# Kernel tuning notes

Measured on AMD Instinct MI355X. Metric: run time of the kernel, lower is better.

## Reference

```python
import jax, jax.numpy as jnp
import numpy as np

D, H, HD, P, IMG, GRID = 768, 12, 64, 16, 224, 14
L = GRID * GRID            # 196 patch tokens
S = L + 1                  # +CLS
LAYERS, FF, OUT, N = 12, 3072, 512, 16
MASKING_BLOCK, LAST_LAYER = 10, 10  # returns at block 11 (= last_layer + 1)
NEG = -1e30


def setup_inputs() -> dict:
    key = jax.random.key(0)
    ks = jax.random.split(key, 20)
    nrm = lambda k, shp, s=0.02: jax.random.normal(k, shp, dtype=jnp.float32) * s
    inp = {}
    inp['masked_img'] = jax.random.normal(ks[0], (N, 3, IMG, IMG), jnp.float32)
    inp['prompted_img'] = jax.random.normal(ks[1], (N, 3, IMG, IMG), jnp.float32)
    # binary segmentation masks (match torch bool-cast semantics in make_attn_mask)
    inp['pred_masks'] = (jax.random.uniform(ks[2], (N, GRID, GRID)) > 0.5).astype(jnp.float32)
    inp['conv_w'] = nrm(ks[3], (D, 3, P, P))
    inp['class_emb'] = nrm(ks[4], (D,))
    inp['pos_emb'] = nrm(ks[5], (S, D))
    inp['ln_pre_g'] = jnp.ones((D,), jnp.float32)
    inp['ln_pre_b'] = jnp.zeros((D,), jnp.float32)
    inp['Wqkv'] = nrm(ks[6], (LAYERS, 3 * D, D))
    inp['bqkv'] = jnp.zeros((LAYERS, 3 * D), jnp.float32)
    inp['Wo'] = nrm(ks[7], (LAYERS, D, D))
    inp['bo'] = jnp.zeros((LAYERS, D), jnp.float32)
    inp['ln1_g'] = jnp.ones((LAYERS, D), jnp.float32)
    inp['ln1_b'] = jnp.zeros((LAYERS, D), jnp.float32)
    inp['ln2_g'] = jnp.ones((LAYERS, D), jnp.float32)
    inp['ln2_b'] = jnp.zeros((LAYERS, D), jnp.float32)
    inp['Wfc'] = nrm(ks[8], (LAYERS, FF, D))
    inp['bfc'] = jnp.zeros((LAYERS, FF), jnp.float32)
    inp['Wp'] = nrm(ks[9], (LAYERS, D, FF))
    inp['bp'] = jnp.zeros((LAYERS, D), jnp.float32)
    inp['ln_post_g'] = jnp.ones((D,), jnp.float32)
    inp['ln_post_b'] = jnp.zeros((D,), jnp.float32)
    inp['proj'] = nrm(ks[10], (D, OUT))
    return inp


def _ln(x, g, b, eps=1e-5):
    mu = jnp.mean(x, axis=-1, keepdims=True)
    var = jnp.mean(jnp.square(x - mu), axis=-1, keepdims=True)
    return (x - mu) * jax.lax.rsqrt(var + eps) * g + b


def _mha(x, Wqkv, bqkv, Wo, bo, bias=None):
    B, Sx, _ = x.shape
    qkv = x @ Wqkv.T + bqkv
    q, k, v = jnp.split(qkv, 3, axis=-1)
    q = q.reshape(B, Sx, H, HD)
    k = k.reshape(B, Sx, H, HD)
    v = v.reshape(B, Sx, H, HD)
    scores = jnp.einsum('bqhd,bkhd->bhqk', q, k) / jnp.sqrt(jnp.float32(HD))
    if bias is not None:
        scores = scores + bias  # bias: [B,1,S,S] broadcast over heads
    a = jax.nn.softmax(scores, axis=-1)
    o = jnp.einsum('bhqk,bkhd->bqhd', a, v).reshape(B, Sx, D)
    return o @ Wo.T + bo


def _embed(img, conv_w, class_emb, pos_emb, ln_pre_g, ln_pre_b):
    feat = jax.lax.conv_general_dilated(
        img, conv_w, window_strides=(P, P), padding='VALID',
        dimension_numbers=('NCHW', 'OIHW', 'NCHW'))  # [B,D,14,14]
    tok = feat.reshape(img.shape[0], D, L).transpose(0, 2, 1)  # [B,L,D]
    cls = jnp.broadcast_to(class_emb, (img.shape[0], 1, D))
    x = jnp.concatenate([cls, tok], axis=1) + pos_emb
    return _ln(x, ln_pre_g, ln_pre_b)


def reference(masked_img, prompted_img, pred_masks, conv_w, class_emb, pos_emb,
              ln_pre_g, ln_pre_b, Wqkv, bqkv, Wo, bo, ln1_g, ln1_b, ln2_g, ln2_b,
              Wfc, bfc, Wp, bp, ln_post_g, ln_post_b, proj):
    def block(x, i, bias=None):
        x = x + _mha(_ln(x, ln1_g[i], ln1_b[i]), Wqkv[i], bqkv[i], Wo[i], bo[i], bias)
        h = _ln(x, ln2_g[i], ln2_b[i]) @ Wfc[i].T + bfc[i]
        h = h * jax.nn.sigmoid(1.702 * h)  # QuickGELU
        return x + h @ Wp[i].T + bp[i]

    x = _embed(masked_img, conv_w, class_emb, pos_emb, ln_pre_g, ln_pre_b)
    x2 = _embed(prompted_img, conv_w, class_emb, pos_emb, ln_pre_g, ln_pre_b)
    x12 = jnp.concatenate([x, x2], axis=0)  # share blocks over both streams
    for i in range(MASKING_BLOCK):
        x12 = block(x12, i)
    n = pred_masks.shape[0]
    x, x2 = x12[:n], x12[n:]
    pm = pred_masks.reshape(n, L, 1)
    # attn mask: only CLS row masked where pred_mask == 0 (True in ~attn_masks -> -inf)
    cls_bias = jnp.where(pred_masks.reshape(n, L) != 0, 0.0, NEG)
    bias = jnp.zeros((n, 1, S, S), jnp.float32).at[:, 0, 0, 1:].set(cls_bias)
    for i in (MASKING_BLOCK, LAST_LAYER + 1):  # blocks 10, 11
        _x2 = jnp.concatenate([x2[:, :1, :], x2[:, 1:, :] * pm], axis=1)  # token masking
        x = block(_x2 * 2.0 + x, i)
        x2 = block(x2, i, bias)
    cls_out = _ln(x[:, 0], ln_post_g, ln_post_b)
    return cls_out @ proj  # [N, 512]
```

## Files before the change

kernel.cpp:

```cpp
#include <hip/hip_runtime.h>
#include <cstdint>
#include <cstddef>

#define D_ 768
#define NH_ 12
#define HD_ 64
#define S_ 197
#define LTOK_ 196
#define FF_ 3072
#define NIMG_ 16
#define OUT_ 512
#define LAYERS_ 12

typedef unsigned short u16;
typedef __bf16 bf16x8 __attribute__((ext_vector_type(8)));
typedef float f32x4 __attribute__((ext_vector_type(4)));
typedef u16 u16x8 __attribute__((ext_vector_type(8)));

__device__ __forceinline__ u16 f2bf(float f) {
  uint32_t u = __builtin_bit_cast(uint32_t, f);
  u = (u + 0x7FFFu + ((u >> 16) & 1u)) >> 16;
  return (u16)u;
}

typedef __attribute__((address_space(3))) void lvoid;
typedef __attribute__((address_space(1))) void gvoid;
__device__ __forceinline__ void async16(const u16* g, u16* l) {
  __builtin_amdgcn_global_load_lds((gvoid*)(uintptr_t)g,
                                   (lvoid*)(uint32_t)(uintptr_t)l, 16, 0, 0);
}

__global__ __launch_bounds__(256) void cvt_kernel(const float* __restrict__ src,
                                                  u16* __restrict__ dst, int n4) {
  int i = blockIdx.x * 256 + threadIdx.x;
  if (i >= n4) return;
  const float4 v = ((const float4*)src)[i];
  ushort4 o;
  o.x = f2bf(v.x); o.y = f2bf(v.y); o.z = f2bf(v.z); o.w = f2bf(v.w);
  ((ushort4*)dst)[i] = o;
}

__global__ __launch_bounds__(256) void im2col_kernel(const float* __restrict__ mimg,
                                                     const float* __restrict__ pimg,
                                                     u16* __restrict__ Xp) {
  const int row = blockIdx.x;
  const int n = row / LTOK_, l = row % LTOK_;
  const float* img = (n < NIMG_) ? (mimg + (size_t)n * 3 * 224 * 224)
                                 : (pimg + (size_t)(n - NIMG_) * 3 * 224 * 224);
  const int gy = l / 14, gx = l % 14;
  for (int col = threadIdx.x; col < D_; col += 256) {
    const int c = col >> 8, py = (col >> 4) & 15, px = col & 15;
    Xp[(size_t)row * D_ + col] = f2bf(img[c * 50176 + (gy * 16 + py) * 224 + gx * 16 + px]);
  }
}

template <int EPI>
__global__ __launch_bounds__(256, 2) void gemm_bt(const u16* __restrict__ A,
                                                  const u16* __restrict__ Bw,
                                                  const float* __restrict__ bias,
                                                  float* __restrict__ Cf,
                                                  u16* __restrict__ Cb,
                                                  int M, int N, int K) {
  __shared__ __align__(16) u16 As[128 * 32];
  __shared__ __align__(16) u16 Bs[128 * 32];
  const int t = threadIdx.x, lane = t & 63, w = t >> 6;
  const int wm = (w >> 1) << 6, wn = (w & 1) << 6;
  const int mBase = blockIdx.y << 7, nBase = blockIdx.x << 7;
  f32x4 acc[4][4];
  const f32x4 z = {0.f, 0.f, 0.f, 0.f};
#pragma unroll
  for (int i = 0; i < 4; i++)
#pragma unroll
    for (int j = 0; j < 4; j++) acc[i][j] = z;

  const int lr = t >> 2, lc = (t & 3) << 3;
  const u16* Ag = A + (size_t)(mBase + lr) * K + lc;
  const u16* Bg = Bw + (size_t)(nBase + lr) * K + lc;
  const size_t halfs = (size_t)64 * K;
  u16* Al = As + t * 8;
  u16* Bl = Bs + t * 8;
  const int q8 = (lane >> 4) << 3, r16 = lane & 15;

  for (int k0 = 0; k0 < K; k0 += 32) {
    async16(Ag, Al);  async16(Ag + halfs, Al + 2048);
    async16(Bg, Bl);  async16(Bg + halfs, Bl + 2048);
    Ag += 32; Bg += 32;
    __syncthreads();
    bf16x8 af[4], bfr[4];
#pragma unroll
    for (int mt = 0; mt < 4; mt++)
      af[mt] = *(const bf16x8*)(As + (wm + mt * 16 + r16) * 32 + q8);
#pragma unroll
    for (int nt = 0; nt < 4; nt++)
      bfr[nt] = *(const bf16x8*)(Bs + (wn + nt * 16 + r16) * 32 + q8);
#pragma unroll
    for (int mt = 0; mt < 4; mt++)
#pragma unroll
      for (int nt = 0; nt < 4; nt++)
        acc[mt][nt] = __builtin_amdgcn_mfma_f32_16x16x32_bf16(af[mt], bfr[nt], acc[mt][nt], 0, 0, 0);
    __syncthreads();
  }

  const int colB = nBase + wn + r16;
  const int rowB = mBase + wm + ((lane >> 4) << 2);
#pragma unroll
  for (int nt = 0; nt < 4; nt++) {
    const int col = colB + nt * 16;
    const float bv = (EPI == 0) ? 0.f : bias[col];
#pragma unroll
    for (int mt = 0; mt < 4; mt++) {
#pragma unroll
      for (int r = 0; r < 4; r++) {
        const int row = rowB + mt * 16 + r;
        const size_t o = (size_t)row * N + col;
        const float v = acc[mt][nt][r];
        if (EPI == 0) {
          Cf[o] = v;
        } else if (EPI == 1) {
          Cb[o] = f2bf(v + bv);
        } else if (EPI == 2) {
          const float hh = v + bv;
          Cb[o] = f2bf(hh / (1.f + __expf(-1.702f * hh)));
        } else {
          Cf[o] += v + bv;
        }
      }
    }
  }
}

__device__ __forceinline__ void st_ln(float* p, float v) { *p = v; }
__device__ __forceinline__ void st_ln(u16* p, float v) { *p = f2bf(v); }

template <typename OT>
__global__ __launch_bounds__(256) void ln_rows(const float* __restrict__ x, size_t strideIn,
                                               OT* __restrict__ y, size_t strideOut,
                                               const float* __restrict__ gw,
                                               const float* __restrict__ bw) {
  const int row = blockIdx.x, t = threadIdx.x;
  const float* xr = x + (size_t)row * strideIn;
  float v0 = xr[t], v1 = xr[t + 256], v2 = xr[t + 512];
  float s1 = v0 + v1 + v2;
  float s2 = v0 * v0 + v1 * v1 + v2 * v2;
#pragma unroll
  for (int off = 1; off < 64; off <<= 1) {
    s1 += __shfl_xor(s1, off);
    s2 += __shfl_xor(s2, off);
  }
  __shared__ float as1[4], as2[4];
  const int lane = t & 63, w = t >> 6;
  if (lane == 0) { as1[w] = s1; as2[w] = s2; }
  __syncthreads();
  s1 = as1[0] + as1[1] + as1[2] + as1[3];
  s2 = as2[0] + as2[1] + as2[2] + as2[3];
  const float mu = s1 * (1.f / 768.f);
  const float rs = rsqrtf(fmaxf(s2 * (1.f / 768.f) - mu * mu, 0.f) + 1e-5f);
  OT* yr = y + (size_t)row * strideOut;
  st_ln(yr + t, (v0 - mu) * rs * gw[t] + bw[t]);
  st_ln(yr + t + 256, (v1 - mu) * rs * gw[t + 256] + bw[t + 256]);
  st_ln(yr + t + 512, (v2 - mu) * rs * gw[t + 512] + bw[t + 512]);
}

__global__ __launch_bounds__(256) void assemble_x(const float* __restrict__ tokf,
                                                  const float* __restrict__ cls,
                                                  const float* __restrict__ pos,
                                                  float* __restrict__ x12) {
  const int row = blockIdx.x;
  const int n = row / S_, s = row % S_;
  for (int d = threadIdx.x; d < D_; d += 256) {
    float v = (s == 0) ? cls[d] : tokf[(size_t)(n * LTOK_ + s - 1) * D_ + d];
    x12[(size_t)row * D_ + d] = v + pos[s * D_ + d];
  }
}

__global__ __launch_bounds__(256) void combine_kernel(float* __restrict__ xa,
                                                      const float* __restrict__ xb,
                                                      const float* __restrict__ pm) {
  const int row = blockIdx.x;
  const int b = row / S_, s = row % S_;
  const float m2 = (s == 0) ? 2.f : 2.f * pm[b * LTOK_ + s - 1];
  for (int d = threadIdx.x; d < D_; d += 256) {
    const size_t o = (size_t)row * D_ + d;
    xa[o] += m2 * xb[o];
  }
}

#define KPAD_ 224
#define VSTR_ 232

__global__ __launch_bounds__(256, 2) void attn_kernel(const u16* __restrict__ qkv,
                                                      u16* __restrict__ out,
                                                      const float* __restrict__ pm,
                                                      int useBias) {
  __shared__ __align__(16) u16 Vt[64 * VSTR_];
  __shared__ __align__(16) u16 Pb4[4 * 16 * VSTR_];
  const int bh = blockIdx.x, b = bh / NH_, h = bh % NH_;
  const int t = threadIdx.x, lane = t & 63, w = t >> 6;
  const int r16 = lane & 15, quad = lane >> 4;

  const u16* Qb = qkv + (size_t)b * S_ * 2304 + h * HD_;
  const u16* Kb = Qb + D_;
  const u16* Vb = Qb + 2 * D_;

#pragma unroll
  for (int it = 0; it < 7; it++) {
    const int lin = it * 256 + t;
    const int col = lin & 63, k0 = (lin >> 6) << 3;
    u16x8 tmp;
#pragma unroll
    for (int j = 0; j < 8; j++) {
      const int key = k0 + j;
      tmp[j] = (key < S_) ? Vb[(size_t)key * 2304 + col] : (u16)0;
    }
    *(u16x8*)&Vt[col * VSTR_ + k0] = tmp;
  }
  __syncthreads();

  u16* Pb = Pb4 + w * (16 * VSTR_);
  const f32x4 z = {0.f, 0.f, 0.f, 0.f};

  for (int it = 0; it < 4; it++) {
    int mt = it * 4 + w;
    const bool real = (mt < 13);
    if (!real) mt = 12;
    const int qbase = mt * 16;

    const u16* qrow = Qb + (size_t)(qbase + r16) * 2304 + quad * 8;
    const bf16x8 a0 = *(const bf16x8*)(qrow);
    const bf16x8 a1 = *(const bf16x8*)(qrow + 32);
    f32x4 c[14];
#pragma unroll
    for (int nt = 0; nt < 14; nt++) {
      const u16* krow = Kb + (size_t)(nt * 16 + r16) * 2304 + quad * 8;
      const bf16x8 b0 = *(const bf16x8*)(krow);
      const bf16x8 b1 = *(const bf16x8*)(krow + 32);
      f32x4 cc = __builtin_amdgcn_mfma_f32_16x16x32_bf16(a0, b0, z, 0, 0, 0);
      c[nt] = __builtin_amdgcn_mfma_f32_16x16x32_bf16(a1, b1, cc, 0, 0, 0);
    }

    float mx[4] = {-3.0e38f, -3.0e38f, -3.0e38f, -3.0e38f};
#pragma unroll
    for (int nt = 0; nt < 14; nt++) {
      const int key = nt * 16 + r16;
      if (key >= S_) {
#pragma unroll
        for (int r = 0; r < 4; r++) c[nt][r] = -1e30f;
      } else {
#pragma unroll
        for (int r = 0; r < 4; r++) c[nt][r] *= 0.125f;
        if (useBias && mt == 0 && quad == 0 && key >= 1)
          c[nt][0] += (pm[b * LTOK_ + key - 1] != 0.f) ? 0.f : -1e30f;
      }
#pragma unroll
      for (int r = 0; r < 4; r++) mx[r] = fmaxf(mx[r], c[nt][r]);
    }
#pragma unroll
    for (int off = 1; off < 16; off <<= 1)
#pragma unroll
      for (int r = 0; r < 4; r++) mx[r] = fmaxf(mx[r], __shfl_xor(mx[r], off));
    float sum[4] = {0.f, 0.f, 0.f, 0.f};
#pragma unroll
    for (int nt = 0; nt < 14; nt++)
#pragma unroll
      for (int r = 0; r < 4; r++) {
        const float e = __expf(c[nt][r] - mx[r]);
        c[nt][r] = e;
        sum[r] += e;
      }
#pragma unroll
    for (int off = 1; off < 16; off <<= 1)
#pragma unroll
      for (int r = 0; r < 4; r++) sum[r] += __shfl_xor(sum[r], off);
    float inv[4];
#pragma unroll
    for (int r = 0; r < 4; r++) inv[r] = 1.f / sum[r];

#pragma unroll
    for (int nt = 0; nt < 14; nt++)
#pragma unroll
      for (int r = 0; r < 4; r++)
        Pb[(quad * 4 + r) * VSTR_ + nt * 16 + r16] = f2bf(c[nt][r] * inv[r]);
    __syncthreads();

    f32x4 ov[4] = {z, z, z, z};
#pragma unroll
    for (int kk = 0; kk < 7; kk++) {
      const bf16x8 pa = *(const bf16x8*)(Pb + r16 * VSTR_ + kk * 32 + quad * 8);
#pragma unroll
      for (int vt = 0; vt < 4; vt++) {
        const bf16x8 vb = *(const bf16x8*)(Vt + (vt * 16 + r16) * VSTR_ + kk * 32 + quad * 8);
        ov[vt] = __builtin_amdgcn_mfma_f32_16x16x32_bf16(pa, vb, ov[vt], 0, 0, 0);
      }
    }
    if (real) {
#pragma unroll
      for (int r = 0; r < 4; r++) {
        const int qq = qbase + quad * 4 + r;
        if (qq < S_) {
#pragma unroll
          for (int vt = 0; vt < 4; vt++)
            out[(size_t)(b * S_ + qq) * D_ + h * HD_ + vt * 16 + r16] = f2bf(ov[vt][r]);
        }
      }
    }
    __syncthreads();
  }
}

__global__ __launch_bounds__(256) void final_proj_kernel(const float* __restrict__ clsn,
                                                         const float* __restrict__ proj,
                                                         float* __restrict__ outp) {
  __shared__ float cs[D_];
  const int b = blockIdx.x;
  for (int d = threadIdx.x; d < D_; d += 256) cs[d] = clsn[b * D_ + d];
  __syncthreads();
  for (int o = threadIdx.x; o < OUT_; o += 256) {
    float acc = 0.f;
    for (int d = 0; d < D_; d++) acc += cs[d] * proj[d * OUT_ + o];
    outp[b * OUT_ + o] = acc;
  }
}

extern "C" void kernel_launch(void* const* d_in, const int* in_sizes, int n_in,
                              void* d_out, int out_size, void* d_ws, size_t ws_size,
                              hipStream_t stream) {
  (void)in_sizes; (void)n_in; (void)out_size; (void)ws_size;
  const float* masked   = (const float*)d_in[0];
  const float* prompted = (const float*)d_in[1];
  const float* pmasks   = (const float*)d_in[2];
  const float* conv_w   = (const float*)d_in[3];
  const float* class_emb= (const float*)d_in[4];
  const float* pos_emb  = (const float*)d_in[5];
  const float* ln_pre_g = (const float*)d_in[6];
  const float* ln_pre_b = (const float*)d_in[7];
  const float* Wqkv     = (const float*)d_in[8];
  const float* bqkv     = (const float*)d_in[9];
  const float* Wo       = (const float*)d_in[10];
  const float* bo       = (const float*)d_in[11];
  const float* ln1_g    = (const float*)d_in[12];
  const float* ln1_b    = (const float*)d_in[13];
  const float* ln2_g    = (const float*)d_in[14];
  const float* ln2_b    = (const float*)d_in[15];
  const float* Wfc      = (const float*)d_in[16];
  const float* bfc      = (const float*)d_in[17];
  const float* Wp       = (const float*)d_in[18];
  const float* bp       = (const float*)d_in[19];
  const float* ln_post_g= (const float*)d_in[20];
  const float* ln_post_b= (const float*)d_in[21];
  const float* projw    = (const float*)d_in[22];

  char* pws = (char*)d_ws;
  auto take = [&](size_t bytes) { char* r = pws; pws += (bytes + 255) & ~(size_t)255; return r; };
  u16*   wqkv_all = (u16*)take((size_t)LAYERS_ * 2304 * D_ * 2);
  u16*   wo_all   = (u16*)take((size_t)LAYERS_ * D_ * D_ * 2);
  u16*   wfc_all  = (u16*)take((size_t)LAYERS_ * FF_ * D_ * 2);
  u16*   wp_all   = (u16*)take((size_t)LAYERS_ * D_ * FF_ * 2);
  u16*   wc       = (u16*)take((size_t)D_ * D_ * 2);
  u16*   Xp       = (u16*)take((size_t)6272 * D_ * 2);
  float* tokf     = (float*)take((size_t)6272 * D_ * 4);
  float* x12      = (float*)take((size_t)6400 * D_ * 4);
  u16*   xn       = (u16*)take((size_t)6400 * D_ * 2);
  u16*   qkvb     = (u16*)take((size_t)6400 * 2304 * 2);
  u16*   ao       = (u16*)take((size_t)6400 * D_ * 2);
  u16*   hb       = (u16*)take((size_t)6400 * FF_ * 2);
  float* xa       = (float*)take((size_t)3200 * D_ * 4);
  float* xb       = (float*)take((size_t)3200 * D_ * 4);
  float* clsn     = (float*)take((size_t)16 * D_ * 4);

  auto cvt = [&](const float* s, u16* d, size_t n) {
    int n4 = (int)(n >> 2);
    cvt_kernel<<<dim3((n4 + 255) / 256), dim3(256), 0, stream>>>(s, d, n4);
  };
  cvt(Wqkv,   wqkv_all, (size_t)LAYERS_ * 2304 * D_);
  cvt(Wo,     wo_all,   (size_t)LAYERS_ * D_ * D_);
  cvt(Wfc,    wfc_all,  (size_t)LAYERS_ * FF_ * D_);
  cvt(Wp,     wp_all,   (size_t)LAYERS_ * D_ * FF_);
  cvt(conv_w, wc,       (size_t)D_ * D_);

  im2col_kernel<<<dim3(6272), dim3(256), 0, stream>>>(masked, prompted, Xp);
  gemm_bt<0><<<dim3(6, 49), dim3(256), 0, stream>>>(Xp, wc, nullptr, tokf, nullptr, 6272, D_, D_);
  assemble_x<<<dim3(32 * S_), dim3(256), 0, stream>>>(tokf, class_emb, pos_emb, x12);
  ln_rows<float><<<dim3(32 * S_), dim3(256), 0, stream>>>(x12, D_, x12, D_, ln_pre_g, ln_pre_b);

  auto run_block = [&](float* x, int Mp, int Mv, int Batt, int li, int useBias) {
    const int gy = Mp / 128;
    ln_rows<u16><<<dim3(Mv), dim3(256), 0, stream>>>(x, D_, xn, D_, ln1_g + li * D_, ln1_b + li * D_);
    gemm_bt<1><<<dim3(18, gy), dim3(256), 0, stream>>>(
        xn, wqkv_all + (size_t)li * 2304 * D_, bqkv + li * 2304, nullptr, qkvb, Mp, 2304, D_);
    attn_kernel<<<dim3(Batt * NH_), dim3(256), 0, stream>>>(qkvb, ao, pmasks, useBias);
    gemm_bt<3><<<dim3(6, gy), dim3(256), 0, stream>>>(
        ao, wo_all + (size_t)li * D_ * D_, bo + li * D_, x, nullptr, Mp, D_, D_);
    ln_rows<u16><<<dim3(Mv), dim3(256), 0, stream>>>(x, D_, xn, D_, ln2_g + li * D_, ln2_b + li * D_);
    gemm_bt<2><<<dim3(24, gy), dim3(256), 0, stream>>>(
        xn, wfc_all + (size_t)li * FF_ * D_, bfc + li * FF_, nullptr, hb, Mp, FF_, D_);
    gemm_bt<3><<<dim3(6, gy), dim3(256), 0, stream>>>(
        hb, wp_all + (size_t)li * D_ * FF_, bp + li * D_, x, nullptr, Mp, D_, FF_);
  };

  for (int li = 0; li < 10; li++) run_block(x12, 6400, 32 * S_, 32, li, 0);

  hipMemcpyAsync(xa, x12, (size_t)NIMG_ * S_ * D_ * 4, hipMemcpyDeviceToDevice, stream);
  hipMemcpyAsync(xb, x12 + (size_t)NIMG_ * S_ * D_, (size_t)NIMG_ * S_ * D_ * 4,
                 hipMemcpyDeviceToDevice, stream);

  for (int li = 10; li <= 11; li++) {
    combine_kernel<<<dim3(NIMG_ * S_), dim3(256), 0, stream>>>(xa, xb, pmasks);
    run_block(xa, 3200, NIMG_ * S_, NIMG_, li, 0);
    run_block(xb, 3200, NIMG_ * S_, NIMG_, li, 1);
  }

  ln_rows<float><<<dim3(16), dim3(256), 0, stream>>>(xa, (size_t)S_ * D_, clsn, D_,
                                                     ln_post_g, ln_post_b);
  final_proj_kernel<<<dim3(16), dim3(256), 0, stream>>>(clsn, projw, (float*)d_out);
}
```

Measured before the change: 3.877 ms.

## Load 64-wide K slabs per barrier and swizzle GEMM blocks into row panels

The GEMM now stages two 32-wide K slices into separate LDS buffers per iteration, halving the number of barrier pairs and issuing more async loads before each wait. The launch grid becomes 1D, and block ids are remapped into panels of 8 row-tiles so that neighbouring blocks share A and B tiles in L2. This doubles LDS per block and assumes K is a multiple of 64, which holds for 768 and 3072.

```diff
diff --git a/kernel.cpp b/kernel.cpp
--- a/kernel.cpp
+++ b/kernel.cpp
@@ -60,12 +60,23 @@
                                                   const float* __restrict__ bias,
                                                   float* __restrict__ Cf,
                                                   u16* __restrict__ Cb,
-                                                  int M, int N, int K) {
-  __shared__ __align__(16) u16 As[128 * 32];
-  __shared__ __align__(16) u16 Bs[128 * 32];
+                                                  int M, int N, int K,
+                                                  int gxN, int gyN) {
+  __shared__ __align__(16) u16 As[2][128 * 32];
+  __shared__ __align__(16) u16 Bs[2][128 * 32];
   const int t = threadIdx.x, lane = t & 63, w = t >> 6;
   const int wm = (w >> 1) << 6, wn = (w & 1) << 6;
-  const int mBase = blockIdx.y << 7, nBase = blockIdx.x << 7;
+
+  const int id = blockIdx.x;
+  const int panelBlocks = gxN << 3;
+  const int p = id / panelBlocks;
+  const int lid = id - p * panelBlocks;
+  const int prm = gyN - (p << 3);
+  const int pr = prm < 8 ? prm : 8;
+  const int gy = (p << 3) + lid % pr;
+  const int gx = lid / pr;
+  const int mBase = gy << 7, nBase = gx << 7;
+
   f32x4 acc[4][4];
   const f32x4 z = {0.f, 0.f, 0.f, 0.f};
 #pragma unroll
@@ -77,27 +88,32 @@
   const u16* Ag = A + (size_t)(mBase + lr) * K + lc;
   const u16* Bg = Bw + (size_t)(nBase + lr) * K + lc;
   const size_t halfs = (size_t)64 * K;
-  u16* Al = As + t * 8;
-  u16* Bl = Bs + t * 8;
+  u16* Al0 = As[0] + t * 8;  u16* Al1 = As[1] + t * 8;
+  u16* Bl0 = Bs[0] + t * 8;  u16* Bl1 = Bs[1] + t * 8;
   const int q8 = (lane >> 4) << 3, r16 = lane & 15;
 
-  for (int k0 = 0; k0 < K; k0 += 32) {
-    async16(Ag, Al);  async16(Ag + halfs, Al + 2048);
-    async16(Bg, Bl);  async16(Bg + halfs, Bl + 2048);
-    Ag += 32; Bg += 32;
+  for (int k0 = 0; k0 < K; k0 += 64) {
+    async16(Ag,          Al0);  async16(Ag + halfs,      Al0 + 2048);
+    async16(Ag + 32,     Al1);  async16(Ag + 32 + halfs, Al1 + 2048);
+    async16(Bg,          Bl0);  async16(Bg + halfs,      Bl0 + 2048);
+    async16(Bg + 32,     Bl1);  async16(Bg + 32 + halfs, Bl1 + 2048);
+    Ag += 64; Bg += 64;
     __syncthreads();
-    bf16x8 af[4], bfr[4];
-#pragma unroll
-    for (int mt = 0; mt < 4; mt++)
-      af[mt] = *(const bf16x8*)(As + (wm + mt * 16 + r16) * 32 + q8);
-#pragma unroll
-    for (int nt = 0; nt < 4; nt++)
-      bfr[nt] = *(const bf16x8*)(Bs + (wn + nt * 16 + r16) * 32 + q8);
-#pragma unroll
-    for (int mt = 0; mt < 4; mt++)
+#pragma unroll
+    for (int kh = 0; kh < 2; kh++) {
+      bf16x8 af[4], bfr[4];
+#pragma unroll
+      for (int mt = 0; mt < 4; mt++)
+        af[mt] = *(const bf16x8*)(As[kh] + (wm + mt * 16 + r16) * 32 + q8);
 #pragma unroll
       for (int nt = 0; nt < 4; nt++)
-        acc[mt][nt] = __builtin_amdgcn_mfma_f32_16x16x32_bf16(af[mt], bfr[nt], acc[mt][nt], 0, 0, 0);
+        bfr[nt] = *(const bf16x8*)(Bs[kh] + (wn + nt * 16 + r16) * 32 + q8);
+#pragma unroll
+      for (int mt = 0; mt < 4; mt++)
+#pragma unroll
+        for (int nt = 0; nt < 4; nt++)
+          acc[mt][nt] = __builtin_amdgcn_mfma_f32_16x16x32_bf16(af[mt], bfr[nt], acc[mt][nt], 0, 0, 0);
+    }
     __syncthreads();
   }
 
@@ -185,7 +201,6 @@
   }
 }
 
-#define KPAD_ 224
 #define VSTR_ 232
 
 __global__ __launch_bounds__(256, 2) void attn_kernel(const u16* __restrict__ qkv,
@@ -378,23 +393,28 @@
   cvt(conv_w, wc,       (size_t)D_ * D_);
 
   im2col_kernel<<<dim3(6272), dim3(256), 0, stream>>>(masked, prompted, Xp);
-  gemm_bt<0><<<dim3(6, 49), dim3(256), 0, stream>>>(Xp, wc, nullptr, tokf, nullptr, 6272, D_, D_);
+  gemm_bt<0><<<dim3(6 * 49), dim3(256), 0, stream>>>(Xp, wc, nullptr, tokf, nullptr,
+                                                     6272, D_, D_, 6, 49);
   assemble_x<<<dim3(32 * S_), dim3(256), 0, stream>>>(tokf, class_emb, pos_emb, x12);
   ln_rows<float><<<dim3(32 * S_), dim3(256), 0, stream>>>(x12, D_, x12, D_, ln_pre_g, ln_pre_b);
 
   auto run_block = [&](float* x, int Mp, int Mv, int Batt, int li, int useBias) {
     const int gy = Mp / 128;
     ln_rows<u16><<<dim3(Mv), dim3(256), 0, stream>>>(x, D_, xn, D_, ln1_g + li * D_, ln1_b + li * D_);
-    gemm_bt<1><<<dim3(18, gy), dim3(256), 0, stream>>>(
-        xn, wqkv_all + (size_t)li * 2304 * D_, bqkv + li * 2304, nullptr, qkvb, Mp, 2304, D_);
+    gemm_bt<1><<<dim3(18 * gy), dim3(256), 0, stream>>>(
+        xn, wqkv_all + (size_t)li * 2304 * D_, bqkv + li * 2304, nullptr, qkvb,
+        Mp, 2304, D_, 18, gy);
     attn_kernel<<<dim3(Batt * NH_), dim3(256), 0, stream>>>(qkvb, ao, pmasks, useBias);
-    gemm_bt<3><<<dim3(6, gy), dim3(256), 0, stream>>>(
-        ao, wo_all + (size_t)li * D_ * D_, bo + li * D_, x, nullptr, Mp, D_, D_);
+    gemm_bt<3><<<dim3(6 * gy), dim3(256), 0, stream>>>(
+        ao, wo_all + (size_t)li * D_ * D_, bo + li * D_, x, nullptr,
+        Mp, D_, D_, 6, gy);
     ln_rows<u16><<<dim3(Mv), dim3(256), 0, stream>>>(x, D_, xn, D_, ln2_g + li * D_, ln2_b + li * D_);
-    gemm_bt<2><<<dim3(24, gy), dim3(256), 0, stream>>>(
-        xn, wfc_all + (size_t)li * FF_ * D_, bfc + li * FF_, nullptr, hb, Mp, FF_, D_);
-    gemm_bt<3><<<dim3(6, gy), dim3(256), 0, stream>>>(
-        hb, wp_all + (size_t)li * D_ * FF_, bp + li * D_, x, nullptr, Mp, D_, FF_);
+    gemm_bt<2><<<dim3(24 * gy), dim3(256), 0, stream>>>(
+        xn, wfc_all + (size_t)li * FF_ * D_, bfc + li * FF_, nullptr, hb,
+        Mp, FF_, D_, 24, gy);
+    gemm_bt<3><<<dim3(6 * gy), dim3(256), 0, stream>>>(
+        hb, wp_all + (size_t)li * D_ * FF_, bp + li * D_, x, nullptr,
+        Mp, D_, FF_, 6, gy);
   };
 
   for (int li = 0; li < 10; li++) run_block(x12, 6400, 32 * S_, 32, li, 0);
```

Result: faster. 3.498 ms (-9.8%).
